# Kernel tuning notes

Hardware: AMD Instinct MI355X
Metric: run time of the kernel (lower is better)

Reference implementation:

```python
import jax, jax.numpy as jnp
import numpy as np

NEG_SLOPE = 0.2  # PyG GATConv default negative_slope


def gat_conv(x, edge_index, W, att_src, att_dst, bias, heads, out_ch):
    """PyG GATConv (eval mode): add self loops, per-head linear, edge attention,
    per-destination softmax, weighted scatter-sum, concat heads, add bias."""
    N = x.shape[0]
    loops = jnp.arange(N, dtype=edge_index.dtype)
    src = jnp.concatenate([edge_index[0], loops])  # [E+N]
    dst = jnp.concatenate([edge_index[1], loops])
    h = (x @ W).reshape(N, heads, out_ch)                      # [N,H,C]
    a_src = jnp.einsum('nhc,hc->nh', h, att_src)               # [N,H]
    a_dst = jnp.einsum('nhc,hc->nh', h, att_dst)
    alpha = jax.nn.leaky_relu(a_src[src] + a_dst[dst], NEG_SLOPE)  # [E,H]
    # numerically stable segment softmax over edges grouped by dst node
    amax = jax.ops.segment_max(alpha, dst, num_segments=N)     # [N,H]
    e = jnp.exp(alpha - amax[dst])
    denom = jax.ops.segment_sum(e, dst, num_segments=N)
    alpha = e / (denom[dst] + 1e-16)
    msg = h[src] * alpha[:, :, None]                           # [E,H,C]
    out = jax.ops.segment_sum(msg, dst, num_segments=N)        # [N,H,C]
    return out.reshape(N, heads * out_ch) + bias


def setup_inputs() -> dict:
    key = jax.random.key(0)
    ks = jax.random.split(key, 12)
    N, F_IN, F_OUT = 50000, 512, 128
    E = 800000
    H1, C1 = 8, 8  # conv1: heads=8, 8 channels per head -> 64 concat
    x = jax.random.normal(ks[0], (N, F_IN), dtype=jnp.float32)
    edge_index = jax.random.randint(ks[1], (2, E), 0, N, dtype=jnp.int64)
    s1 = 1.0 / np.sqrt(F_IN)
    s2 = 1.0 / np.sqrt(H1 * C1)
    W1 = jax.random.normal(ks[2], (F_IN, H1 * C1), dtype=jnp.float32) * s1
    att_src1 = jax.random.normal(ks[3], (H1, C1), dtype=jnp.float32) * s2
    att_dst1 = jax.random.normal(ks[4], (H1, C1), dtype=jnp.float32) * s2
    b1 = jnp.zeros((H1 * C1,), dtype=jnp.float32)
    W2 = jax.random.normal(ks[5], (H1 * C1, F_OUT), dtype=jnp.float32) * s2
    att_src2 = jax.random.normal(ks[6], (1, F_OUT), dtype=jnp.float32) * (1.0 / np.sqrt(F_OUT))
    att_dst2 = jax.random.normal(ks[7], (1, F_OUT), dtype=jnp.float32) * (1.0 / np.sqrt(F_OUT))
    b2 = jnp.zeros((F_OUT,), dtype=jnp.float32)
    return {"x": x, "edge_index": edge_index,
            "W1": W1, "att_src1": att_src1, "att_dst1": att_dst1, "b1": b1,
            "W2": W2, "att_src2": att_src2, "att_dst2": att_dst2, "b2": b2}


def reference(x, edge_index, W1, att_src1, att_dst1, b1, W2, att_src2, att_dst2, b2):
    # eval mode: F.dropout(p=0.6, training=False) is identity
    h = gat_conv(x, edge_index, W1, att_src1, att_dst1, b1, heads=8, out_ch=8)
    h = jax.nn.elu(h)
    out = gat_conv(h, edge_index, W2, att_src2, att_dst2, b2, heads=1, out_ch=128)
    return out
```

## Files before the change

### kernel.cpp

```cpp
#include <hip/hip_runtime.h>
#include <cstdint>

typedef __attribute__((ext_vector_type(8))) __bf16 bf16x8;
typedef __attribute__((ext_vector_type(4))) float f32x4;


__global__ __launch_bounds__(256) void k_hist(const int* __restrict__ ei,
        int E, int E2, int* __restrict__ deg) {
    int e = blockIdx.x * 256 + threadIdx.x;
    if (e >= E2) return;
    int dst = (e < E) ? ei[E + e] : (e - E);
    atomicAdd(&deg[dst], 1);
}

__global__ __launch_bounds__(256) void k_scanA(const int* __restrict__ deg,
        int* __restrict__ partials, int N) {
    int t = threadIdx.x;
    int base = blockIdx.x * 2048 + t * 8;
    int s = 0;
    #pragma unroll
    for (int j = 0; j < 8; ++j) { int i = base + j; if (i < N) s += deg[i]; }
    #pragma unroll
    for (int off = 32; off >= 1; off >>= 1) s += __shfl_xor(s, off, 64);
    __shared__ int ws[4];
    if ((t & 63) == 0) ws[t >> 6] = s;
    __syncthreads();
    if (t == 0) partials[blockIdx.x] = ws[0] + ws[1] + ws[2] + ws[3];
}

__global__ __launch_bounds__(64) void k_scanB(int* __restrict__ partials,
        int nb, int* __restrict__ row_start, int N) {
    int lane = threadIdx.x;
    int run = 0;
    for (int b0 = 0; b0 < nb; b0 += 64) {
        int v = (b0 + lane < nb) ? partials[b0 + lane] : 0;
        int s = v;
        #pragma unroll
        for (int d = 1; d < 64; d <<= 1) {
            int u = __shfl_up(s, d, 64);
            if (lane >= d) s += u;
        }
        if (b0 + lane < nb) partials[b0 + lane] = run + s - v;
        run += __shfl(s, 63, 64);
    }
    if (lane == 0) row_start[N] = run;
}

__global__ __launch_bounds__(256) void k_scanC(const int* __restrict__ deg,
        const int* __restrict__ partials, int* __restrict__ row_start, int N) {
    int t = threadIdx.x;
    int base = blockIdx.x * 2048 + t * 8;
    int v[8], s = 0;
    #pragma unroll
    for (int j = 0; j < 8; ++j) { int i = base + j; v[j] = (i < N) ? deg[i] : 0; s += v[j]; }
    int lane = t & 63, w = t >> 6;
    int incl = s;
    #pragma unroll
    for (int d = 1; d < 64; d <<= 1) {
        int u = __shfl_up(incl, d, 64);
        if (lane >= d) incl += u;
    }
    __shared__ int wsum[4];
    if (lane == 63) wsum[w] = incl;
    __syncthreads();
    int woff = 0;
    #pragma unroll
    for (int i = 0; i < 4; ++i) if (i < w) woff += wsum[i];
    int run = partials[blockIdx.x] + woff + incl - s;
    #pragma unroll
    for (int j = 0; j < 8; ++j) {
        int i = base + j;
        if (i < N) row_start[i] = run;
        run += v[j];
    }
}

__global__ __launch_bounds__(256) void k_scatter(const int* __restrict__ ei,
        int E, int E2, const int* __restrict__ row_start, int* __restrict__ cursor,
        int* __restrict__ csr_src) {
    int e = blockIdx.x * 256 + threadIdx.x;
    if (e >= E2) return;
    int src, dst;
    if (e < E) { src = ei[e]; dst = ei[E + e]; }
    else       { src = e - E; dst = src; }
    int pos = row_start[dst] + atomicAdd(&cursor[dst], 1);
    csr_src[pos] = src;
}


__global__ __launch_bounds__(256) void k_wconv(const float* __restrict__ W,
        __bf16* __restrict__ Wb) {
    int e = blockIdx.x * 256 + threadIdx.x;
    int k = e >> 6, n = e & 63;
    int s = k >> 5, g = (k >> 3) & 3, j = k & 7;
    int ct = n >> 4;
    int lane = (n & 15) | (g << 4);
    Wb[(((s * 4 + ct) * 64 + lane) << 3) + j] = (__bf16)W[e];
}


__global__ __launch_bounds__(256) void k_gemm1(const float* __restrict__ x,
        const __bf16* __restrict__ Wb, float* __restrict__ h1,
        __bf16* __restrict__ h1b, int N) {
    int t = threadIdx.x;
    int l = t & 63, w = t >> 6;
    int g = l >> 4;
    int arow = blockIdx.x * 64 + w * 16 + (l & 15);
    const float* xbase = x + (size_t)min(arow, N - 1) * 512 + g * 8;

    f32x4 acc[4] = {{0.f,0.f,0.f,0.f},{0.f,0.f,0.f,0.f},
                    {0.f,0.f,0.f,0.f},{0.f,0.f,0.f,0.f}};
    #pragma unroll 4
    for (int s = 0; s < 16; ++s) {
        float4 xa = *(const float4*)(xbase + s * 32);
        float4 xb = *(const float4*)(xbase + s * 32 + 4);
        bf16x8 a;
        a[0] = (__bf16)xa.x; a[1] = (__bf16)xa.y; a[2] = (__bf16)xa.z; a[3] = (__bf16)xa.w;
        a[4] = (__bf16)xb.x; a[5] = (__bf16)xb.y; a[6] = (__bf16)xb.z; a[7] = (__bf16)xb.w;
        #pragma unroll
        for (int ct = 0; ct < 4; ++ct) {
            bf16x8 b = *reinterpret_cast<const bf16x8*>(Wb + (((s * 4 + ct) * 64 + l) << 3));
            acc[ct] = __builtin_amdgcn_mfma_f32_16x16x32_bf16(a, b, acc[ct], 0, 0, 0);
        }
    }
    int orow0 = blockIdx.x * 64 + w * 16 + g * 4;
    #pragma unroll
    for (int ct = 0; ct < 4; ++ct) {
        int col = ct * 16 + (l & 15);
        #pragma unroll
        for (int r = 0; r < 4; ++r) {
            int row = orow0 + r;
            if (row < N) {
                float v = acc[ct][r];
                h1[(size_t)row * 64 + col] = v;
                h1b[(size_t)row * 64 + col] = (__bf16)v;
            }
        }
    }
}


__global__ __launch_bounds__(256) void k_gemm2(const float* __restrict__ hin,
        const float* __restrict__ W, float* __restrict__ h2,
        __bf16* __restrict__ h2b, int N) {
    __shared__ float xs[64][65];
    __shared__ float ws[64][128];
    int t = threadIdx.x;
    int row0 = blockIdx.x * 64;
    #pragma unroll
    for (int u = 0; u < 4; ++u) {
        int idx = t + u * 256;
        int r = idx >> 4, f = idx & 15;
        int grow = row0 + r;
        float4 v = make_float4(0.f, 0.f, 0.f, 0.f);
        if (grow < N) v = *(const float4*)(hin + (size_t)grow * 64 + f * 4);
        xs[r][f * 4 + 0] = v.x; xs[r][f * 4 + 1] = v.y;
        xs[r][f * 4 + 2] = v.z; xs[r][f * 4 + 3] = v.w;
    }
    #pragma unroll
    for (int u = 0; u < 8; ++u) {
        int idx = t + u * 256;
        int kr = idx >> 5, c4 = (idx & 31) * 4;
        *(float4*)&ws[kr][c4] = *(const float4*)(W + (size_t)kr * 128 + c4);
    }
    __syncthreads();
    int c0 = (t & 15) * 8;
    int r0 = (t >> 4) * 4;
    float4 acc[4][2] = {};
    #pragma unroll 8
    for (int kk = 0; kk < 64; ++kk) {
        float4 w0 = *(const float4*)&ws[kk][c0];
        float4 w1 = *(const float4*)&ws[kk][c0 + 4];
        #pragma unroll
        for (int i = 0; i < 4; ++i) {
            float a = xs[r0 + i][kk];
            acc[i][0].x += a * w0.x; acc[i][0].y += a * w0.y;
            acc[i][0].z += a * w0.z; acc[i][0].w += a * w0.w;
            acc[i][1].x += a * w1.x; acc[i][1].y += a * w1.y;
            acc[i][1].z += a * w1.z; acc[i][1].w += a * w1.w;
        }
    }
    #pragma unroll
    for (int i = 0; i < 4; ++i) {
        int row = row0 + r0 + i;
        if (row < N) {
            *(float4*)(h2 + (size_t)row * 128 + c0) = acc[i][0];
            *(float4*)(h2 + (size_t)row * 128 + c0 + 4) = acc[i][1];
            bf16x8 hb;
            hb[0] = (__bf16)acc[i][0].x; hb[1] = (__bf16)acc[i][0].y;
            hb[2] = (__bf16)acc[i][0].z; hb[3] = (__bf16)acc[i][0].w;
            hb[4] = (__bf16)acc[i][1].x; hb[5] = (__bf16)acc[i][1].y;
            hb[6] = (__bf16)acc[i][1].z; hb[7] = (__bf16)acc[i][1].w;
            *(bf16x8*)(h2b + (size_t)row * 128 + c0) = hb;
        }
    }
}


__global__ __launch_bounds__(256) void k_att1(const float* __restrict__ h1,
        const float* __restrict__ att_src, const float* __restrict__ att_dst,
        float* __restrict__ a_s, float* __restrict__ a_d, int NH) {
    int i = blockIdx.x * 256 + threadIdx.x;
    if (i >= NH) return;
    int h = i & 7;
    const float* hp = h1 + (size_t)i * 8;
    const float* sp = att_src + h * 8;
    const float* dp = att_dst + h * 8;
    float s = 0.f, d = 0.f;
    #pragma unroll
    for (int c = 0; c < 8; ++c) { float v = hp[c]; s += v * sp[c]; d += v * dp[c]; }
    a_s[i] = s; a_d[i] = d;
}

__global__ __launch_bounds__(256) void k_att2(const float* __restrict__ h2,
        const float* __restrict__ att_src, const float* __restrict__ att_dst,
        float* __restrict__ a_s, float* __restrict__ a_d, int N) {
    int node = blockIdx.x * 4 + (threadIdx.x >> 6);
    int lane = threadIdx.x & 63;
    if (node >= N) return;
    const float* hp = h2 + (size_t)node * 128;
    float v0 = hp[lane], v1 = hp[lane + 64];
    float s = v0 * att_src[lane] + v1 * att_src[lane + 64];
    float d = v0 * att_dst[lane] + v1 * att_dst[lane + 64];
    #pragma unroll
    for (int off = 32; off >= 1; off >>= 1) {
        s += __shfl_xor(s, off, 64);
        d += __shfl_xor(d, off, 64);
    }
    if (lane == 0) { a_s[node] = s; a_d[node] = d; }
}


__global__ __launch_bounds__(256) void k_gat1(
        const int* __restrict__ row_start, const int* __restrict__ csr_src,
        const __bf16* __restrict__ h1b,
        const float* __restrict__ a_src, const float* __restrict__ a_dst,
        const float* __restrict__ bias, float* __restrict__ outp, int N) {
    int node = blockIdx.x * 4 + (threadIdx.x >> 6);
    int lane = threadIdx.x & 63;
    if (node >= N) return;
    int j = lane >> 3, c = lane & 7;
    int start = row_start[node], end = row_start[node + 1];
    float adc = a_dst[(size_t)node * 8 + c];

    float acc[8] = {};
    float wsum = 0.f;
    #pragma unroll 2
    for (int base = start; base < end; base += 8) {
        int idx = base + j;
        if (idx < end) {
            int s = csr_src[idx];
            float a = a_src[(size_t)s * 8 + c] + adc;
            a = a > 0.f ? a : 0.2f * a;
            float w = __expf(a);
            wsum += w;
            bf16x8 v = *(const bf16x8*)(h1b + (size_t)s * 64 + c * 8);
            #pragma unroll
            for (int e = 0; e < 8; ++e) acc[e] = fmaf(w, (float)v[e], acc[e]);
        }
    }
    #pragma unroll
    for (int off = 8; off <= 32; off <<= 1) {
        wsum += __shfl_xor(wsum, off, 64);
        #pragma unroll
        for (int e = 0; e < 8; ++e) acc[e] += __shfl_xor(acc[e], off, 64);
    }
    if (j == 0) {
        float inv = 1.f / (wsum + 1e-16f);
        float* op = outp + (size_t)node * 64 + c * 8;
        const float* bp = bias + c * 8;
        #pragma unroll
        for (int e = 0; e < 8; ++e) {
            float v = acc[e] * inv + bp[e];
            op[e] = v > 0.f ? v : __expf(v) - 1.f;
        }
    }
}


__global__ __launch_bounds__(256) void k_gat2(
        const int* __restrict__ row_start, const int* __restrict__ csr_src,
        const __bf16* __restrict__ h2b,
        const float* __restrict__ a_src, const float* __restrict__ a_dst,
        const float* __restrict__ bias, float* __restrict__ outp, int N) {
    int node = blockIdx.x * 4 + (threadIdx.x >> 6);
    int lane = threadIdx.x & 63;
    if (node >= N) return;
    int j = lane >> 4, c = lane & 15;
    int start = row_start[node], end = row_start[node + 1];
    float adst = a_dst[node];

    float acc[8] = {};
    float wsum = 0.f;
    #pragma unroll 2
    for (int base = start; base < end; base += 4) {
        int idx = base + j;
        if (idx < end) {
            int s = csr_src[idx];
            float a = a_src[s] + adst;
            a = a > 0.f ? a : 0.2f * a;
            float w = __expf(a);
            wsum += w;
            bf16x8 v = *(const bf16x8*)(h2b + (size_t)s * 128 + c * 8);
            #pragma unroll
            for (int e = 0; e < 8; ++e) acc[e] = fmaf(w, (float)v[e], acc[e]);
        }
    }
    #pragma unroll
    for (int off = 16; off <= 32; off <<= 1) {
        wsum += __shfl_xor(wsum, off, 64);
        #pragma unroll
        for (int e = 0; e < 8; ++e) acc[e] += __shfl_xor(acc[e], off, 64);
    }
    if (j == 0) {
        float inv = 1.f / (wsum + 1e-16f);
        float* op = outp + (size_t)node * 128 + c * 8;
        const float* bp = bias + c * 8;
        #pragma unroll
        for (int e = 0; e < 8; ++e)
            op[e] = acc[e] * inv + bp[e];
    }
}


extern "C" void kernel_launch(void* const* d_in, const int* in_sizes, int n_in,
                              void* d_out, int out_size, void* d_ws, size_t ws_size,
                              hipStream_t stream) {
    const float* x   = (const float*)d_in[0];
    const int*   ei  = (const int*)d_in[1];
    const float* W1  = (const float*)d_in[2];
    const float* as1 = (const float*)d_in[3];
    const float* ad1 = (const float*)d_in[4];
    const float* b1  = (const float*)d_in[5];
    const float* W2  = (const float*)d_in[6];
    const float* as2 = (const float*)d_in[7];
    const float* ad2 = (const float*)d_in[8];
    const float* b2  = (const float*)d_in[9];
    int N  = in_sizes[0] / 512;
    int E  = in_sizes[1] / 2;
    int E2 = E + N;

    char* wsp = (char*)d_ws;
    size_t off = 0;
    auto alloc = [&](size_t bytes) {
        char* p = wsp + off;
        off = (off + bytes + 255) & ~(size_t)255;
        return p;
    };
    float*  h1   = (float*)alloc((size_t)N * 64 * 4);
    __bf16* h1b  = (__bf16*)alloc((size_t)N * 64 * 2);
    float*  hmid = (float*)alloc((size_t)N * 64 * 4);
    float*  h2   = (float*)alloc((size_t)N * 128 * 4);
    __bf16* h2b  = (__bf16*)alloc((size_t)N * 128 * 2);
    float*  a1s  = (float*)alloc((size_t)N * 8 * 4);
    float*  a1d  = (float*)alloc((size_t)N * 8 * 4);
    float*  a2s  = (float*)alloc((size_t)N * 4);
    float*  a2d  = (float*)alloc((size_t)N * 4);
    __bf16* Wb1  = (__bf16*)alloc((size_t)512 * 64 * 2);
    int* deg    = (int*)alloc((size_t)2 * N * 4);
    int* cursor = deg + N;
    int* row_start = (int*)alloc((size_t)(N + 1) * 4);
    int* csr_src   = (int*)alloc((size_t)E2 * 4);
    int nbscan = (N + 2047) / 2048;
    int* partials  = (int*)alloc((size_t)nbscan * 4);
    (void)ws_size; (void)n_in; (void)out_size;

    hipMemsetAsync(deg, 0, (size_t)2 * N * 4, stream);
    int eb = (E2 + 255) / 256;
    k_hist<<<eb, 256, 0, stream>>>(ei, E, E2, deg);
    k_scanA<<<nbscan, 256, 0, stream>>>(deg, partials, N);
    k_scanB<<<1, 64, 0, stream>>>(partials, nbscan, row_start, N);
    k_scanC<<<nbscan, 256, 0, stream>>>(deg, partials, row_start, N);
    k_scatter<<<eb, 256, 0, stream>>>(ei, E, E2, row_start, cursor, csr_src);

    int gb64 = (N + 63) / 64;
    int nb4 = (N + 3) / 4;
    k_wconv<<<128, 256, 0, stream>>>(W1, Wb1);
    k_gemm1<<<gb64, 256, 0, stream>>>(x, Wb1, h1, h1b, N);
    k_att1<<<(N * 8 + 255) / 256, 256, 0, stream>>>(h1, as1, ad1, a1s, a1d, N * 8);
    k_gat1<<<nb4, 256, 0, stream>>>(row_start, csr_src, h1b, a1s, a1d, b1, hmid, N);
    k_gemm2<<<gb64, 256, 0, stream>>>(hmid, W2, h2, h2b, N);
    k_att2<<<nb4, 256, 0, stream>>>(h2, as2, ad2, a2s, a2d, N);
    k_gat2<<<nb4, 256, 0, stream>>>(row_start, csr_src, h2b, a2s, a2d, b2, (float*)d_out, N);
}
```

Before: 225.4 us.

## Split-K gemm1, MFMA gemm2 with fused attention, bf16 intermediates, merged scan

Several changes land together. The scanB kernel is removed, and each scanC block now sums the partials before it. gemm1 is split into two K-halves to double the block count, and the halves are summed in att1, which also writes the bf16 copy of h1. gat1 now writes its ELU output as bf16. gemm2 is rewritten to use MFMA on bf16 inputs and computes the layer-2 attention scores in its epilogue, which removes att2 and the fp32 h2 buffer. The aim is fewer launches, less memory traffic and better GPU occupancy, at the cost of extra partial-sum traffic and lower precision in the intermediates.

```diff
diff --git a/kernel.cpp b/kernel.cpp
--- a/kernel.cpp
+++ b/kernel.cpp
@@ -28,28 +28,14 @@
     if (t == 0) partials[blockIdx.x] = ws[0] + ws[1] + ws[2] + ws[3];
 }
 
-__global__ __launch_bounds__(64) void k_scanB(int* __restrict__ partials,
-        int nb, int* __restrict__ row_start, int N) {
-    int lane = threadIdx.x;
-    int run = 0;
-    for (int b0 = 0; b0 < nb; b0 += 64) {
-        int v = (b0 + lane < nb) ? partials[b0 + lane] : 0;
-        int s = v;
-        #pragma unroll
-        for (int d = 1; d < 64; d <<= 1) {
-            int u = __shfl_up(s, d, 64);
-            if (lane >= d) s += u;
-        }
-        if (b0 + lane < nb) partials[b0 + lane] = run + s - v;
-        run += __shfl(s, 63, 64);
-    }
-    if (lane == 0) row_start[N] = run;
-}
-
 __global__ __launch_bounds__(256) void k_scanC(const int* __restrict__ deg,
-        const int* __restrict__ partials, int* __restrict__ row_start, int N) {
+        const int* __restrict__ partials, int* __restrict__ row_start,
+        int N, int nb) {
     int t = threadIdx.x;
-    int base = blockIdx.x * 2048 + t * 8;
+    int bid = blockIdx.x;
+    int boff = 0;
+    for (int b = 0; b < bid; ++b) boff += partials[b];
+    int base = bid * 2048 + t * 8;
     int v[8], s = 0;
     #pragma unroll
     for (int j = 0; j < 8; ++j) { int i = base + j; v[j] = (i < N) ? deg[i] : 0; s += v[j]; }
@@ -66,12 +52,17 @@
     int woff = 0;
     #pragma unroll
     for (int i = 0; i < 4; ++i) if (i < w) woff += wsum[i];
-    int run = partials[blockIdx.x] + woff + incl - s;
+    int run = boff + woff + incl - s;
     #pragma unroll
     for (int j = 0; j < 8; ++j) {
         int i = base + j;
         if (i < N) row_start[i] = run;
         run += v[j];
+    }
+    if (bid == 0 && t == 0) {
+        int tot = 0;
+        for (int b = 0; b < nb; ++b) tot += partials[b];
+        row_start[N] = tot;
     }
 }
 
@@ -88,30 +79,43 @@
 }
 
 
-__global__ __launch_bounds__(256) void k_wconv(const float* __restrict__ W,
-        __bf16* __restrict__ Wb) {
+__global__ __launch_bounds__(256) void k_wconv(const float* __restrict__ W1,
+        const float* __restrict__ W2, __bf16* __restrict__ Wb1,
+        __bf16* __restrict__ Wb2) {
     int e = blockIdx.x * 256 + threadIdx.x;
-    int k = e >> 6, n = e & 63;
-    int s = k >> 5, g = (k >> 3) & 3, j = k & 7;
-    int ct = n >> 4;
-    int lane = (n & 15) | (g << 4);
-    Wb[(((s * 4 + ct) * 64 + lane) << 3) + j] = (__bf16)W[e];
+    if (e < 32768) {
+        int k = e >> 6, n = e & 63;
+        int s = k >> 5, g = (k >> 3) & 3, j = k & 7;
+        int ct = n >> 4;
+        int lane = (n & 15) | (g << 4);
+        Wb1[(((s * 4 + ct) * 64 + lane) << 3) + j] = (__bf16)W1[e];
+    } else {
+        int e2 = e - 32768;
+        int k = e2 >> 7, n = e2 & 127;
+        int s = k >> 5, g = (k >> 3) & 3, j = k & 7;
+        int ct = n >> 4;
+        int lane = (n & 15) | (g << 4);
+        Wb2[(((s * 8 + ct) * 64 + lane) << 3) + j] = (__bf16)W2[e2];
+    }
 }
 
 
 __global__ __launch_bounds__(256) void k_gemm1(const float* __restrict__ x,
-        const __bf16* __restrict__ Wb, float* __restrict__ h1,
-        __bf16* __restrict__ h1b, int N) {
+        const __bf16* __restrict__ Wb, float* __restrict__ h1p, int N) {
+    int bid = blockIdx.x;
+    int half = bid & 1, tile = bid >> 1;
     int t = threadIdx.x;
     int l = t & 63, w = t >> 6;
     int g = l >> 4;
-    int arow = blockIdx.x * 64 + w * 16 + (l & 15);
+    int arow = tile * 64 + w * 16 + (l & 15);
     const float* xbase = x + (size_t)min(arow, N - 1) * 512 + g * 8;
 
     f32x4 acc[4] = {{0.f,0.f,0.f,0.f},{0.f,0.f,0.f,0.f},
                     {0.f,0.f,0.f,0.f},{0.f,0.f,0.f,0.f}};
+    int s0 = half * 8;
     #pragma unroll 4
-    for (int s = 0; s < 16; ++s) {
+    for (int si = 0; si < 8; ++si) {
+        int s = s0 + si;
         float4 xa = *(const float4*)(xbase + s * 32);
         float4 xb = *(const float4*)(xbase + s * 32 + 4);
         bf16x8 a;
@@ -123,111 +127,46 @@
             acc[ct] = __builtin_amdgcn_mfma_f32_16x16x32_bf16(a, b, acc[ct], 0, 0, 0);
         }
     }
-    int orow0 = blockIdx.x * 64 + w * 16 + g * 4;
+    float* hp = h1p + (size_t)half * N * 64;
+    int orow0 = tile * 64 + w * 16 + g * 4;
     #pragma unroll
     for (int ct = 0; ct < 4; ++ct) {
         int col = ct * 16 + (l & 15);
         #pragma unroll
         for (int r = 0; r < 4; ++r) {
             int row = orow0 + r;
-            if (row < N) {
-                float v = acc[ct][r];
-                h1[(size_t)row * 64 + col] = v;
-                h1b[(size_t)row * 64 + col] = (__bf16)v;
-            }
-        }
-    }
-}
-
-
-__global__ __launch_bounds__(256) void k_gemm2(const float* __restrict__ hin,
-        const float* __restrict__ W, float* __restrict__ h2,
-        __bf16* __restrict__ h2b, int N) {
-    __shared__ float xs[64][65];
-    __shared__ float ws[64][128];
-    int t = threadIdx.x;
-    int row0 = blockIdx.x * 64;
-    #pragma unroll
-    for (int u = 0; u < 4; ++u) {
-        int idx = t + u * 256;
-        int r = idx >> 4, f = idx & 15;
-        int grow = row0 + r;
-        float4 v = make_float4(0.f, 0.f, 0.f, 0.f);
-        if (grow < N) v = *(const float4*)(hin + (size_t)grow * 64 + f * 4);
-        xs[r][f * 4 + 0] = v.x; xs[r][f * 4 + 1] = v.y;
-        xs[r][f * 4 + 2] = v.z; xs[r][f * 4 + 3] = v.w;
-    }
-    #pragma unroll
-    for (int u = 0; u < 8; ++u) {
-        int idx = t + u * 256;
-        int kr = idx >> 5, c4 = (idx & 31) * 4;
-        *(float4*)&ws[kr][c4] = *(const float4*)(W + (size_t)kr * 128 + c4);
-    }
-    __syncthreads();
-    int c0 = (t & 15) * 8;
-    int r0 = (t >> 4) * 4;
-    float4 acc[4][2] = {};
-    #pragma unroll 8
-    for (int kk = 0; kk < 64; ++kk) {
-        float4 w0 = *(const float4*)&ws[kk][c0];
-        float4 w1 = *(const float4*)&ws[kk][c0 + 4];
-        #pragma unroll
-        for (int i = 0; i < 4; ++i) {
-            float a = xs[r0 + i][kk];
-            acc[i][0].x += a * w0.x; acc[i][0].y += a * w0.y;
-            acc[i][0].z += a * w0.z; acc[i][0].w += a * w0.w;
-            acc[i][1].x += a * w1.x; acc[i][1].y += a * w1.y;
-            acc[i][1].z += a * w1.z; acc[i][1].w += a * w1.w;
-        }
-    }
-    #pragma unroll
-    for (int i = 0; i < 4; ++i) {
-        int row = row0 + r0 + i;
-        if (row < N) {
-            *(float4*)(h2 + (size_t)row * 128 + c0) = acc[i][0];
-            *(float4*)(h2 + (size_t)row * 128 + c0 + 4) = acc[i][1];
-            bf16x8 hb;
-            hb[0] = (__bf16)acc[i][0].x; hb[1] = (__bf16)acc[i][0].y;
-            hb[2] = (__bf16)acc[i][0].z; hb[3] = (__bf16)acc[i][0].w;
-            hb[4] = (__bf16)acc[i][1].x; hb[5] = (__bf16)acc[i][1].y;
-            hb[6] = (__bf16)acc[i][1].z; hb[7] = (__bf16)acc[i][1].w;
-            *(bf16x8*)(h2b + (size_t)row * 128 + c0) = hb;
-        }
-    }
-}
-
-
-__global__ __launch_bounds__(256) void k_att1(const float* __restrict__ h1,
+            if (row < N) hp[(size_t)row * 64 + col] = acc[ct][r];
+        }
+    }
+}
+
+
+__global__ __launch_bounds__(256) void k_att1(const float* __restrict__ h1p,
         const float* __restrict__ att_src, const float* __restrict__ att_dst,
-        float* __restrict__ a_s, float* __restrict__ a_d, int NH) {
+        float* __restrict__ a_s, float* __restrict__ a_d,
+        __bf16* __restrict__ h1b, int N) {
     int i = blockIdx.x * 256 + threadIdx.x;
+    int NH = N * 8;
     if (i >= NH) return;
     int h = i & 7;
-    const float* hp = h1 + (size_t)i * 8;
+    const float* p0 = h1p + (size_t)i * 8;
+    const float* p1 = h1p + (size_t)N * 64 + (size_t)i * 8;
+    float4 a0 = *(const float4*)p0,       a1 = *(const float4*)(p0 + 4);
+    float4 b0 = *(const float4*)p1,       b1 = *(const float4*)(p1 + 4);
+    float v[8] = { a0.x + b0.x, a0.y + b0.y, a0.z + b0.z, a0.w + b0.w,
+                   a1.x + b1.x, a1.y + b1.y, a1.z + b1.z, a1.w + b1.w };
     const float* sp = att_src + h * 8;
     const float* dp = att_dst + h * 8;
     float s = 0.f, d = 0.f;
-    #pragma unroll
-    for (int c = 0; c < 8; ++c) { float v = hp[c]; s += v * sp[c]; d += v * dp[c]; }
+    bf16x8 hb;
+    #pragma unroll
+    for (int c = 0; c < 8; ++c) {
+        s += v[c] * sp[c];
+        d += v[c] * dp[c];
+        hb[c] = (__bf16)v[c];
+    }
     a_s[i] = s; a_d[i] = d;
-}
-
-__global__ __launch_bounds__(256) void k_att2(const float* __restrict__ h2,
-        const float* __restrict__ att_src, const float* __restrict__ att_dst,
-        float* __restrict__ a_s, float* __restrict__ a_d, int N) {
-    int node = blockIdx.x * 4 + (threadIdx.x >> 6);
-    int lane = threadIdx.x & 63;
-    if (node >= N) return;
-    const float* hp = h2 + (size_t)node * 128;
-    float v0 = hp[lane], v1 = hp[lane + 64];
-    float s = v0 * att_src[lane] + v1 * att_src[lane + 64];
-    float d = v0 * att_dst[lane] + v1 * att_dst[lane + 64];
-    #pragma unroll
-    for (int off = 32; off >= 1; off >>= 1) {
-        s += __shfl_xor(s, off, 64);
-        d += __shfl_xor(d, off, 64);
-    }
-    if (lane == 0) { a_s[node] = s; a_d[node] = d; }
+    *(bf16x8*)(h1b + (size_t)i * 8) = hb;
 }
 
 
@@ -235,7 +174,7 @@
         const int* __restrict__ row_start, const int* __restrict__ csr_src,
         const __bf16* __restrict__ h1b,
         const float* __restrict__ a_src, const float* __restrict__ a_dst,
-        const float* __restrict__ bias, float* __restrict__ outp, int N) {
+        const float* __restrict__ bias, __bf16* __restrict__ outp, int N) {
     int node = blockIdx.x * 4 + (threadIdx.x >> 6);
     int lane = threadIdx.x & 63;
     if (node >= N) return;
@@ -267,12 +206,69 @@
     }
     if (j == 0) {
         float inv = 1.f / (wsum + 1e-16f);
-        float* op = outp + (size_t)node * 64 + c * 8;
         const float* bp = bias + c * 8;
+        bf16x8 ob;
         #pragma unroll
         for (int e = 0; e < 8; ++e) {
             float v = acc[e] * inv + bp[e];
-            op[e] = v > 0.f ? v : __expf(v) - 1.f;
+            v = v > 0.f ? v : __expf(v) - 1.f;
+            ob[e] = (__bf16)v;
+        }
+        *(bf16x8*)(outp + (size_t)node * 64 + c * 8) = ob;
+    }
+}
+
+
+__global__ __launch_bounds__(256) void k_gemm2(const __bf16* __restrict__ hb,
+        const __bf16* __restrict__ Wb, const float* __restrict__ att_src,
+        const float* __restrict__ att_dst, __bf16* __restrict__ h2b,
+        float* __restrict__ a2s, float* __restrict__ a2d, int N) {
+    int t = threadIdx.x;
+    int l = t & 63, w = t >> 6;
+    int g = l >> 4;
+    int arow = blockIdx.x * 64 + w * 16 + (l & 15);
+    const __bf16* abase = hb + (size_t)min(arow, N - 1) * 64 + g * 8;
+
+    bf16x8 a0 = *(const bf16x8*)(abase);
+    bf16x8 a1 = *(const bf16x8*)(abase + 32);
+    f32x4 acc[8];
+    #pragma unroll
+    for (int ct = 0; ct < 8; ++ct) acc[ct] = (f32x4){0.f,0.f,0.f,0.f};
+    #pragma unroll
+    for (int ct = 0; ct < 8; ++ct) {
+        bf16x8 b0 = *reinterpret_cast<const bf16x8*>(Wb + ((ct * 64 + l) << 3));
+        bf16x8 b1 = *reinterpret_cast<const bf16x8*>(Wb + (((8 + ct) * 64 + l) << 3));
+        acc[ct] = __builtin_amdgcn_mfma_f32_16x16x32_bf16(a0, b0, acc[ct], 0, 0, 0);
+        acc[ct] = __builtin_amdgcn_mfma_f32_16x16x32_bf16(a1, b1, acc[ct], 0, 0, 0);
+    }
+    int orow0 = blockIdx.x * 64 + w * 16 + g * 4;
+    float sp[4] = {0.f,0.f,0.f,0.f}, dp[4] = {0.f,0.f,0.f,0.f};
+    #pragma unroll
+    for (int ct = 0; ct < 8; ++ct) {
+        int col = ct * 16 + (l & 15);
+        float as = att_src[col], ad = att_dst[col];
+        #pragma unroll
+        for (int r = 0; r < 4; ++r) {
+            int row = orow0 + r;
+            float v = acc[ct][r];
+            if (row < N) h2b[(size_t)row * 128 + col] = (__bf16)v;
+            sp[r] = fmaf(v, as, sp[r]);
+            dp[r] = fmaf(v, ad, dp[r]);
+        }
+    }
+    #pragma unroll
+    for (int off = 1; off <= 8; off <<= 1) {
+        #pragma unroll
+        for (int r = 0; r < 4; ++r) {
+            sp[r] += __shfl_xor(sp[r], off, 64);
+            dp[r] += __shfl_xor(dp[r], off, 64);
+        }
+    }
+    if ((l & 15) == 0) {
+        #pragma unroll
+        for (int r = 0; r < 4; ++r) {
+            int row = orow0 + r;
+            if (row < N) { a2s[row] = sp[r]; a2d[row] = dp[r]; }
         }
     }
 }
@@ -347,16 +343,16 @@
         off = (off + bytes + 255) & ~(size_t)255;
         return p;
     };
-    float*  h1   = (float*)alloc((size_t)N * 64 * 4);
-    __bf16* h1b  = (__bf16*)alloc((size_t)N * 64 * 2);
-    float*  hmid = (float*)alloc((size_t)N * 64 * 4);
-    float*  h2   = (float*)alloc((size_t)N * 128 * 4);
-    __bf16* h2b  = (__bf16*)alloc((size_t)N * 128 * 2);
-    float*  a1s  = (float*)alloc((size_t)N * 8 * 4);
-    float*  a1d  = (float*)alloc((size_t)N * 8 * 4);
-    float*  a2s  = (float*)alloc((size_t)N * 4);
-    float*  a2d  = (float*)alloc((size_t)N * 4);
-    __bf16* Wb1  = (__bf16*)alloc((size_t)512 * 64 * 2);
+    float*  h1p   = (float*)alloc((size_t)2 * N * 64 * 4);
+    __bf16* h1b   = (__bf16*)alloc((size_t)N * 64 * 2);
+    __bf16* hmidb = (__bf16*)alloc((size_t)N * 64 * 2);
+    __bf16* h2b   = (__bf16*)alloc((size_t)N * 128 * 2);
+    float*  a1s   = (float*)alloc((size_t)N * 8 * 4);
+    float*  a1d   = (float*)alloc((size_t)N * 8 * 4);
+    float*  a2s   = (float*)alloc((size_t)N * 4);
+    float*  a2d   = (float*)alloc((size_t)N * 4);
+    __bf16* Wb1   = (__bf16*)alloc((size_t)512 * 64 * 2);
+    __bf16* Wb2   = (__bf16*)alloc((size_t)64 * 128 * 2);
     int* deg    = (int*)alloc((size_t)2 * N * 4);
     int* cursor = deg + N;
     int* row_start = (int*)alloc((size_t)(N + 1) * 4);
@@ -369,17 +365,15 @@
     int eb = (E2 + 255) / 256;
     k_hist<<<eb, 256, 0, stream>>>(ei, E, E2, deg);
     k_scanA<<<nbscan, 256, 0, stream>>>(deg, partials, N);
-    k_scanB<<<1, 64, 0, stream>>>(partials, nbscan, row_start, N);
-    k_scanC<<<nbscan, 256, 0, stream>>>(deg, partials, row_start, N);
+    k_scanC<<<nbscan, 256, 0, stream>>>(deg, partials, row_start, N, nbscan);
     k_scatter<<<eb, 256, 0, stream>>>(ei, E, E2, row_start, cursor, csr_src);
 
     int gb64 = (N + 63) / 64;
     int nb4 = (N + 3) / 4;
-    k_wconv<<<128, 256, 0, stream>>>(W1, Wb1);
-    k_gemm1<<<gb64, 256, 0, stream>>>(x, Wb1, h1, h1b, N);
-    k_att1<<<(N * 8 + 255) / 256, 256, 0, stream>>>(h1, as1, ad1, a1s, a1d, N * 8);
-    k_gat1<<<nb4, 256, 0, stream>>>(row_start, csr_src, h1b, a1s, a1d, b1, hmid, N);
-    k_gemm2<<<gb64, 256, 0, stream>>>(hmid, W2, h2, h2b, N);
-    k_att2<<<nb4, 256, 0, stream>>>(h2, as2, ad2, a2s, a2d, N);
+    k_wconv<<<160, 256, 0, stream>>>(W1, W2, Wb1, Wb2);
+    k_gemm1<<<gb64 * 2, 256, 0, stream>>>(x, Wb1, h1p, N);
+    k_att1<<<(N * 8 + 255) / 256, 256, 0, stream>>>(h1p, as1, ad1, a1s, a1d, h1b, N);
+    k_gat1<<<nb4, 256, 0, stream>>>(row_start, csr_src, h1b, a1s, a1d, b1, hmidb, N);
+    k_gemm2<<<gb64, 256, 0, stream>>>(hmidb, Wb2, as2, ad2, h2b, a2s, a2d, N);
     k_gat2<<<nb4, 256, 0, stream>>>(row_start, csr_src, h2b, a2s, a2d, b2, (float*)d_out, N);
 }
```

Measured after the change: 208.5 us, median of 2. 7.5% less time.
